# Kernel optimization log

Hardware: AMD Instinct MI355X
Metric: run time of the kernel (lower is better)

The kernel has to match this reference:

```python
import jax, jax.numpy as jnp
import numpy as np

N_NODES = 100_000
N_EDGES = 1_600_000
N_GRAPHS = 64
IN_CH = 128
HID = 64
OUT_CH = 2


def setup_inputs() -> dict:
    key = jax.random.key(0)
    ks = jax.random.split(key, 12)

    def lin(k, fan_in, fan_out):
        s = 1.0 / np.sqrt(fan_in)
        return jax.random.uniform(k, (fan_in, fan_out), jnp.float32, -s, s)

    x = jax.random.normal(ks[0], (N_NODES, IN_CH), jnp.float32)
    edge_index = jax.random.randint(ks[1], (2, N_EDGES), 0, N_NODES, jnp.int64)
    batch = jnp.sort(jax.random.randint(ks[2], (N_NODES,), 0, N_GRAPHS, jnp.int64))
    return {
        "x": x,
        "edge_index": edge_index,
        "batch": batch,
        "w_rel0": lin(ks[3], IN_CH, HID),
        "b_rel0": jnp.zeros((HID,), jnp.float32),
        "w_root0": lin(ks[4], IN_CH, HID),
        "w_rel1": lin(ks[5], HID, HID),
        "b_rel1": jnp.zeros((HID,), jnp.float32),
        "w_root1": lin(ks[6], HID, HID),
        "w_rel2": lin(ks[7], HID, HID),
        "b_rel2": jnp.zeros((HID,), jnp.float32),
        "w_root2": lin(ks[8], HID, HID),
        "head_w1": lin(ks[9], HID, HID),
        "head_b1": jnp.zeros((HID,), jnp.float32),
        "head_w2": lin(ks[10], HID, OUT_CH),
        "head_b2": jnp.zeros((OUT_CH,), jnp.float32),
    }


def _graph_conv(x, src, dst, w_rel, b_rel, w_root):
    # PyG GraphConv: out = lin_rel(sum_{j->i} x_j) + lin_root(x_i)
    agg = jax.ops.segment_sum(x[src], dst, num_segments=N_NODES)  # [N, d_in]
    return agg @ w_rel + b_rel + x @ w_root


def reference(x, edge_index, batch, w_rel0, b_rel0, w_root0,
              w_rel1, b_rel1, w_root1, w_rel2, b_rel2, w_root2,
              head_w1, head_b1, head_w2, head_b2):
    src, dst = edge_index[0], edge_index[1]
    h = jax.nn.relu(_graph_conv(x, src, dst, w_rel0, b_rel0, w_root0))
    h = jax.nn.relu(_graph_conv(h, src, dst, w_rel1, b_rel1, w_root1))
    h = jax.nn.relu(_graph_conv(h, src, dst, w_rel2, b_rel2, w_root2))
    # global_mean_pool over graph ids (dropout is identity at inference)
    sums = jax.ops.segment_sum(h, batch, num_segments=N_GRAPHS)          # [G, H]
    cnts = jax.ops.segment_sum(jnp.ones((N_NODES,), h.dtype), batch,
                               num_segments=N_GRAPHS)                    # [G]
    pooled = sums / jnp.maximum(cnts, 1.0)[:, None]
    z = jax.nn.relu(pooled @ head_w1 + head_b1)
    return z @ head_w2 + head_b2
```

## Files before the change

kernel.cpp:

```cpp
#include <hip/hip_runtime.h>
#include <hip/hip_bf16.h>

#define CAP 64
#define KBUCK 391
#define BSHIFT 8
#define BCAP 4608
#define CHUNK_A 2048
#define AITER (CHUNK_A / 256)
#define LDSZ 36864

typedef __attribute__((ext_vector_type(8))) short short8;
typedef __attribute__((ext_vector_type(4))) float f32x4;

__device__ inline unsigned short bfbits(float f) {
    __hip_bfloat16 b = __float2bfloat16(f);
    unsigned short u;
    __builtin_memcpy(&u, &b, 2);
    return u;
}

__device__ inline void bucket_body(char* smem, int bb, const int* __restrict__ ei,
                                   int E, int* __restrict__ gcur,
                                   unsigned* __restrict__ bucketed)
{
    int* hist = (int*)smem;
    int* base = hist + KBUCK;
    const int e0 = bb * CHUNK_A;
    const int e1 = min(e0 + CHUNK_A, E);
    for (int i = threadIdx.x; i < KBUCK; i += 256) hist[i] = 0;
    __syncthreads();
    int dreg[AITER];
    #pragma unroll
    for (int it = 0; it < AITER; ++it) {
        int e = e0 + it * 256 + threadIdx.x;
        dreg[it] = (e < e1) ? ei[E + e] : -1;
        if (dreg[it] >= 0) atomicAdd(&hist[dreg[it] >> BSHIFT], 1);
    }
    __syncthreads();
    for (int i = threadIdx.x; i < KBUCK; i += 256) {
        int h = hist[i];
        base[i] = h ? atomicAdd(&gcur[i], h) : 0;
        hist[i] = 0;
    }
    __syncthreads();
    #pragma unroll
    for (int it = 0; it < AITER; ++it) {
        int e = e0 + it * 256 + threadIdx.x;
        if (e < e1) {
            int s = ei[e];
            int d = dreg[it];
            int b = d >> BSHIFT;
            int off = base[b] + atomicAdd(&hist[b], 1);
            if (off < BCAP)
                bucketed[(size_t)b * BCAP + off] = ((unsigned)s << 8) | (unsigned)(d & 255);
        }
    }
}

__global__ __launch_bounds__(256) void build_slots_kernel(
    const unsigned* __restrict__ bucketed, const int* __restrict__ gcur,
    int* __restrict__ cnt, int* __restrict__ slots, int N)
{
    __shared__ int lcnt[256];
    const int b = blockIdx.x;
    const int nb0 = b << BSHIFT;
    lcnt[threadIdx.x] = 0;
    __syncthreads();
    const int count = min(gcur[b], BCAP);
    const unsigned* src = bucketed + (size_t)b * BCAP;
    for (int i = threadIdx.x; i < count; i += 256) {
        unsigned p = src[i];
        int dl = (int)(p & 255u);
        int pos = atomicAdd(&lcnt[dl], 1);
        if (pos < CAP) slots[(size_t)(nb0 + dl) * CAP + pos] = (int)(p >> 8);
    }
    __syncthreads();
    int node = nb0 + threadIdx.x;
    if (node < N) cnt[node] = min(lcnt[threadIdx.x], CAP);
}

__global__ __launch_bounds__(256) void prep_weights_kernel(
    const float* __restrict__ wr0, const float* __restrict__ wt0,
    const float* __restrict__ wr1, const float* __restrict__ wt1,
    const float* __restrict__ wr2, const float* __restrict__ wt2,
    __hip_bfloat16* __restrict__ hi, __hip_bfloat16* __restrict__ lo)
{
    int idx = blockIdx.x * 256 + threadIdx.x;
    if (idx >= 32768) return;
    const float *wr, *wt;
    int n, k;
    if (idx < 16384)      { wr = wr0; wt = wt0; int r = idx;         n = r >> 7; k = r & 127; }
    else if (idx < 24576) { wr = wr1; wt = wt1; int r = idx - 16384; n = r >> 6; k = r & 63; }
    else                  { wr = wr2; wt = wt2; int r = idx - 24576; n = r >> 6; k = r & 63; }
    float w = (n < 64) ? wr[k * 64 + n] : wt[k * 64 + (n - 64)];
    __hip_bfloat16 h = __float2bfloat16(w);
    hi[idx] = h;
    lo[idx] = __float2bfloat16(w - __bfloat162float(h));
}

template <int DIN, bool AFP32>
__device__ inline void mfma_body(
    char* smem, int bx, const void* __restrict__ featv,
    const __hip_bfloat16* __restrict__ whiT, const __hip_bfloat16* __restrict__ wloT,
    const float* __restrict__ b_rel,
    __hip_bfloat16* __restrict__ y, __hip_bfloat16* __restrict__ r, int N)
{
    __hip_bfloat16* As = (__hip_bfloat16*)smem;
    __hip_bfloat16* Bh = As + 128 * 48;
    __hip_bfloat16* Bl = Bh + 128 * 48;
    const int t = threadIdx.x;
    const int lane = t & 63;
    const int wid = t >> 6;
    const int wm = wid >> 1, wn = wid & 1;
    const int node0 = bx * 128;
    const int lrow = lane & 15;
    const int kgrp = lane >> 4;

    f32x4 acc[4][4];
    #pragma unroll
    for (int i = 0; i < 4; ++i)
        #pragma unroll
        for (int j = 0; j < 4; ++j) acc[i][j] = (f32x4){0.f, 0.f, 0.f, 0.f};

    for (int ks = 0; ks < DIN / 32; ++ks) {
        #pragma unroll
        for (int p = 0; p < 2; ++p) {
            int c = t + p * 256;
            int m = c >> 2, kc = c & 3;
            int row = node0 + m; if (row >= N) row = N - 1;
            if (AFP32) {
                const float* feat = (const float*)featv;
                const float* src = feat + (size_t)row * DIN + ks * 32 + kc * 8;
                float4 v0 = *(const float4*)src;
                float4 v1 = *(const float4*)(src + 4);
                union { uint4 q; unsigned short s[8]; } pk;
                pk.s[0] = bfbits(v0.x); pk.s[1] = bfbits(v0.y);
                pk.s[2] = bfbits(v0.z); pk.s[3] = bfbits(v0.w);
                pk.s[4] = bfbits(v1.x); pk.s[5] = bfbits(v1.y);
                pk.s[6] = bfbits(v1.z); pk.s[7] = bfbits(v1.w);
                *(uint4*)&As[m * 48 + kc * 8] = pk.q;
            } else {
                const __hip_bfloat16* feat = (const __hip_bfloat16*)featv;
                *(uint4*)&As[m * 48 + kc * 8] =
                    *(const uint4*)(feat + (size_t)row * DIN + ks * 32 + kc * 8);
            }
        }
        #pragma unroll
        for (int p = 0; p < 4; ++p) {
            int c = t + p * 256;
            int half = c >> 9;
            int cc = c & 511;
            int n = cc >> 2, kc = cc & 3;
            const __hip_bfloat16* w = half ? wloT : whiT;
            uint4 v = *(const uint4*)(w + (size_t)n * DIN + ks * 32 + kc * 8);
            if (half) *(uint4*)&Bl[n * 48 + kc * 8] = v;
            else      *(uint4*)&Bh[n * 48 + kc * 8] = v;
        }
        __syncthreads();

        short8 a[4], bh[4], bl[4];
        #pragma unroll
        for (int i = 0; i < 4; ++i)
            a[i] = *(const short8*)&As[(wm * 64 + i * 16 + lrow) * 48 + kgrp * 8];
        #pragma unroll
        for (int j = 0; j < 4; ++j) {
            bh[j] = *(const short8*)&Bh[(wn * 64 + j * 16 + lrow) * 48 + kgrp * 8];
            bl[j] = *(const short8*)&Bl[(wn * 64 + j * 16 + lrow) * 48 + kgrp * 8];
        }
        #pragma unroll
        for (int i = 0; i < 4; ++i)
            #pragma unroll
            for (int j = 0; j < 4; ++j) {
                acc[i][j] = __builtin_amdgcn_mfma_f32_16x16x32_bf16(a[i], bh[j], acc[i][j], 0, 0, 0);
                acc[i][j] = __builtin_amdgcn_mfma_f32_16x16x32_bf16(a[i], bl[j], acc[i][j], 0, 0, 0);
            }
        __syncthreads();
    }

    #pragma unroll
    for (int i = 0; i < 4; ++i) {
        int mbase = node0 + wm * 64 + i * 16 + kgrp * 4;
        #pragma unroll
        for (int j = 0; j < 4; ++j) {
            int n = wn * 64 + j * 16 + lrow;
            #pragma unroll
            for (int v = 0; v < 4; ++v) {
                int m = mbase + v;
                if (m < N) {
                    float val = acc[i][j][v];
                    if (n < 64) y[(size_t)m * 64 + n] = __float2bfloat16(val);
                    else        r[(size_t)m * 64 + (n - 64)] = __float2bfloat16(val + b_rel[n - 64]);
                }
            }
        }
    }
}

__global__ __launch_bounds__(256) void fused_l0_kernel(
    const float* __restrict__ x,
    const __hip_bfloat16* __restrict__ whiT, const __hip_bfloat16* __restrict__ wloT,
    const float* __restrict__ b_rel,
    __hip_bfloat16* __restrict__ y, __hip_bfloat16* __restrict__ r, int N,
    int gemm_blocks, const int* __restrict__ ei, int E,
    int* __restrict__ gcur, unsigned* __restrict__ bucketed)
{
    extern __shared__ char smem[];
    if ((int)blockIdx.x < gemm_blocks)
        mfma_body<128, true>(smem, blockIdx.x, x, whiT, wloT, b_rel, y, r, N);
    else
        bucket_body(smem, blockIdx.x - gemm_blocks, ei, E, gcur, bucketed);
}

template <int DIN>
__global__ __launch_bounds__(256) void mfma_lin_kernel(
    const __hip_bfloat16* __restrict__ feat,
    const __hip_bfloat16* __restrict__ whiT, const __hip_bfloat16* __restrict__ wloT,
    const float* __restrict__ b_rel,
    __hip_bfloat16* __restrict__ y, __hip_bfloat16* __restrict__ r, int N)
{
    extern __shared__ char smem[];
    mfma_body<DIN, false>(smem, blockIdx.x, feat, whiT, wloT, b_rel, y, r, N);
}

__global__ __launch_bounds__(256) void gather_relu_kernel(
    const __hip_bfloat16* __restrict__ y, const int* __restrict__ cnt,
    const int* __restrict__ slots, const __hip_bfloat16* __restrict__ rin,
    __hip_bfloat16* __restrict__ hout, int N)
{
    const int node = blockIdx.x * 8 + (threadIdx.x >> 5);
    if (node >= N) return;
    const int sub = threadIdx.x & 31;
    const int nb = sub >> 3;
    const int ch = (sub & 7) * 8;
    const int deg = cnt[node];
    const int* sl = slots + (size_t)node * CAP;
    const unsigned short* yp = (const unsigned short*)y;

    float a[8], b[8];
    #pragma unroll
    for (int k = 0; k < 8; ++k) { a[k] = 0.f; b[k] = 0.f; }

    #pragma unroll 2
    for (int j = nb; j < deg; j += 8) {
        int n0 = sl[j];
        uint4 v = *(const uint4*)(yp + (size_t)n0 * 64 + ch);
        a[0] += __uint_as_float(v.x << 16); a[1] += __uint_as_float(v.x & 0xffff0000u);
        a[2] += __uint_as_float(v.y << 16); a[3] += __uint_as_float(v.y & 0xffff0000u);
        a[4] += __uint_as_float(v.z << 16); a[5] += __uint_as_float(v.z & 0xffff0000u);
        a[6] += __uint_as_float(v.w << 16); a[7] += __uint_as_float(v.w & 0xffff0000u);
        int j2 = j + 4;
        if (j2 < deg) {
            int n1 = sl[j2];
            uint4 w = *(const uint4*)(yp + (size_t)n1 * 64 + ch);
            b[0] += __uint_as_float(w.x << 16); b[1] += __uint_as_float(w.x & 0xffff0000u);
            b[2] += __uint_as_float(w.y << 16); b[3] += __uint_as_float(w.y & 0xffff0000u);
            b[4] += __uint_as_float(w.z << 16); b[5] += __uint_as_float(w.z & 0xffff0000u);
            b[6] += __uint_as_float(w.w << 16); b[7] += __uint_as_float(w.w & 0xffff0000u);
        }
    }
    #pragma unroll
    for (int k = 0; k < 8; ++k) {
        a[k] += b[k];
        a[k] += __shfl_xor(a[k], 8);
        a[k] += __shfl_xor(a[k], 16);
    }
    if (nb == 0) {
        uint4 rv = *(const uint4*)((const unsigned short*)rin + (size_t)node * 64 + ch);
        float r0 = __uint_as_float(rv.x << 16), r1 = __uint_as_float(rv.x & 0xffff0000u);
        float r2 = __uint_as_float(rv.y << 16), r3 = __uint_as_float(rv.y & 0xffff0000u);
        float r4 = __uint_as_float(rv.z << 16), r5 = __uint_as_float(rv.z & 0xffff0000u);
        float r6 = __uint_as_float(rv.w << 16), r7 = __uint_as_float(rv.w & 0xffff0000u);
        float f0 = fmaxf(r0 + a[0], 0.f), f1 = fmaxf(r1 + a[1], 0.f);
        float f2 = fmaxf(r2 + a[2], 0.f), f3 = fmaxf(r3 + a[3], 0.f);
        float f4 = fmaxf(r4 + a[4], 0.f), f5 = fmaxf(r5 + a[5], 0.f);
        float f6 = fmaxf(r6 + a[6], 0.f), f7 = fmaxf(r7 + a[7], 0.f);
        union { uint4 q; unsigned short s[8]; } pk;
        pk.s[0] = bfbits(f0); pk.s[1] = bfbits(f1); pk.s[2] = bfbits(f2); pk.s[3] = bfbits(f3);
        pk.s[4] = bfbits(f4); pk.s[5] = bfbits(f5); pk.s[6] = bfbits(f6); pk.s[7] = bfbits(f7);
        *(uint4*)((unsigned short*)hout + (size_t)node * 64 + ch) = pk.q;
    }
}

__global__ __launch_bounds__(256) void pool_kernel(
    const __hip_bfloat16* __restrict__ h, const int* __restrict__ batch,
    float* __restrict__ gsum, int* __restrict__ gcnt, int N)
{
    const int CHUNK = 64;
    int wid = (blockIdx.x * 256 + threadIdx.x) >> 6;
    int lane = threadIdx.x & 63;
    int nb = lane >> 3;
    int ch = (lane & 7) * 8;
    int start = wid * CHUNK;
    if (start >= N) return;
    int end = min(start + CHUNK, N);
    const unsigned short* hp = (const unsigned short*)h;

    float a[8];
    #pragma unroll
    for (int k = 0; k < 8; ++k) a[k] = 0.f;
    int runcnt = 0;
    int i = start;
    int gcur = batch[start];

    while (i < end) {
        int idx = i + lane; if (idx > end - 1) idx = end - 1;
        int bl = batch[idx];
        unsigned long long diff = __ballot(bl != gcur && (i + lane) < end);
        int len = diff ? ((int)__ffsll(diff) - 1) : min(64, end - i);
        for (int j = i + nb; j < i + len; j += 8) {
            uint4 v = *(const uint4*)(hp + (size_t)j * 64 + ch);
            a[0] += __uint_as_float(v.x << 16); a[1] += __uint_as_float(v.x & 0xffff0000u);
            a[2] += __uint_as_float(v.y << 16); a[3] += __uint_as_float(v.y & 0xffff0000u);
            a[4] += __uint_as_float(v.z << 16); a[5] += __uint_as_float(v.z & 0xffff0000u);
            a[6] += __uint_as_float(v.w << 16); a[7] += __uint_as_float(v.w & 0xffff0000u);
        }
        runcnt += len;
        i += len;
        if (diff) {
            #pragma unroll
            for (int k = 0; k < 8; ++k) {
                a[k] += __shfl_xor(a[k], 8);
                a[k] += __shfl_xor(a[k], 16);
                a[k] += __shfl_xor(a[k], 32);
            }
            if (runcnt > 0) {
                if (nb == 0) {
                    #pragma unroll
                    for (int k = 0; k < 8; ++k)
                        atomicAdd(&gsum[gcur * 64 + ch + k], a[k]);
                }
                if (lane == 0) atomicAdd(&gcnt[gcur], runcnt);
            }
            #pragma unroll
            for (int k = 0; k < 8; ++k) a[k] = 0.f;
            runcnt = 0;
            gcur = __shfl(bl, len);
        }
    }
    #pragma unroll
    for (int k = 0; k < 8; ++k) {
        a[k] += __shfl_xor(a[k], 8);
        a[k] += __shfl_xor(a[k], 16);
        a[k] += __shfl_xor(a[k], 32);
    }
    if (runcnt > 0) {
        if (nb == 0) {
            #pragma unroll
            for (int k = 0; k < 8; ++k)
                atomicAdd(&gsum[gcur * 64 + ch + k], a[k]);
        }
        if (lane == 0) atomicAdd(&gcnt[gcur], runcnt);
    }
}

__global__ __launch_bounds__(256) void head_kernel(
    const float* __restrict__ gsum, const int* __restrict__ gcnt,
    const float* __restrict__ w1, const float* __restrict__ b1,
    const float* __restrict__ w2, const float* __restrict__ b2,
    float* __restrict__ out)
{
    __shared__ float pm[64 * 64];
    __shared__ float z[64 * 64];
    int t = threadIdx.x;
    for (int i = t; i < 64 * 64; i += 256) {
        int g = i >> 6;
        float cf = (float)gcnt[g];
        if (cf < 1.f) cf = 1.f;
        pm[i] = gsum[i] / cf;
    }
    __syncthreads();
    for (int i = t; i < 64 * 64; i += 256) {
        int g = i >> 6, c = i & 63;
        float a = b1[c];
        #pragma unroll 8
        for (int k = 0; k < 64; ++k) a = fmaf(pm[g * 64 + k], w1[k * 64 + c], a);
        z[i] = fmaxf(a, 0.f);
    }
    __syncthreads();
    for (int i = t; i < 64 * 2; i += 256) {
        int g = i >> 1, o = i & 1;
        float a = b2[o];
        #pragma unroll 8
        for (int k = 0; k < 64; ++k) a = fmaf(z[g * 64 + k], w2[k * 2 + o], a);
        out[i] = a;
    }
}

extern "C" void kernel_launch(void* const* d_in, const int* in_sizes, int n_in,
                              void* d_out, int out_size, void* d_ws, size_t ws_size,
                              hipStream_t stream)
{
    const float* x       = (const float*)d_in[0];
    const int*   ei      = (const int*)d_in[1];
    const int*   batch   = (const int*)d_in[2];
    const float* w_rel0  = (const float*)d_in[3];
    const float* b_rel0  = (const float*)d_in[4];
    const float* w_root0 = (const float*)d_in[5];
    const float* w_rel1  = (const float*)d_in[6];
    const float* b_rel1  = (const float*)d_in[7];
    const float* w_root1 = (const float*)d_in[8];
    const float* w_rel2  = (const float*)d_in[9];
    const float* b_rel2  = (const float*)d_in[10];
    const float* w_root2 = (const float*)d_in[11];
    const float* hw1     = (const float*)d_in[12];
    const float* hb1     = (const float*)d_in[13];
    const float* hw2     = (const float*)d_in[14];
    const float* hb2     = (const float*)d_in[15];
    float* out = (float*)d_out;

    const int N = in_sizes[0] / 128;
    const int E = in_sizes[1] / 2;
    const int G = 64;

    size_t off = 0;
    auto alloc = [&](size_t bytes) -> void* {
        void* p = (char*)d_ws + off;
        off += (bytes + 255) & ~(size_t)255;
        return p;
    };
    int*      cnt      = (int*)alloc((size_t)N * 4);
    int*      slots    = (int*)alloc((size_t)N * CAP * 4);
    unsigned* bucketed = (unsigned*)alloc((size_t)KBUCK * BCAP * 4);
    int*      gcur     = (int*)alloc((size_t)KBUCK * 4);
    __hip_bfloat16* whiT = (__hip_bfloat16*)alloc(32768 * 2);
    __hip_bfloat16* wloT = (__hip_bfloat16*)alloc(32768 * 2);
    __hip_bfloat16* ybf  = (__hip_bfloat16*)alloc((size_t)N * 64 * 2);
    __hip_bfloat16* h0   = (__hip_bfloat16*)alloc((size_t)N * 64 * 2);
    __hip_bfloat16* h1   = (__hip_bfloat16*)alloc((size_t)N * 64 * 2);
    __hip_bfloat16* rbf  = (__hip_bfloat16*)alloc((size_t)N * 64 * 2);
    float* gsum     = (float*)alloc((size_t)G * 64 * 4);
    int*   gcnt     = (int*)alloc((size_t)G * 4);
    (void)ws_size; (void)n_in;

    hipMemsetAsync(gcur, 0, (size_t)KBUCK * 4, stream);
    hipMemsetAsync(gsum, 0, (size_t)G * 64 * 4, stream);
    hipMemsetAsync(gcnt, 0, (size_t)G * 4, stream);

    prep_weights_kernel<<<128, 256, 0, stream>>>(w_rel0, w_root0, w_rel1, w_root1,
                                                 w_rel2, w_root2, whiT, wloT);

    const int gemm_blocks = (N + 127) / 128;
    const int bucket_blocks = (E + CHUNK_A - 1) / CHUNK_A;
    const int gather_blocks = (N + 7) / 8;

    fused_l0_kernel<<<gemm_blocks + bucket_blocks, 256, LDSZ, stream>>>(
        x, whiT, wloT, b_rel0, ybf, rbf, N, gemm_blocks, ei, E, gcur, bucketed);
    build_slots_kernel<<<KBUCK, 256, 0, stream>>>(bucketed, gcur, cnt, slots, N);
    gather_relu_kernel<<<gather_blocks, 256, 0, stream>>>(ybf, cnt, slots, rbf, h0, N);

    mfma_lin_kernel<64><<<gemm_blocks, 256, LDSZ, stream>>>(
        h0, whiT + 16384, wloT + 16384, b_rel1, ybf, rbf, N);
    gather_relu_kernel<<<gather_blocks, 256, 0, stream>>>(ybf, cnt, slots, rbf, h1, N);

    mfma_lin_kernel<64><<<gemm_blocks, 256, LDSZ, stream>>>(
        h1, whiT + 24576, wloT + 24576, b_rel2, ybf, rbf, N);
    gather_relu_kernel<<<gather_blocks, 256, 0, stream>>>(ybf, cnt, slots, rbf, h0, N);

    int pool_waves  = (N + 63) / 64;
    int pool_blocks = (pool_waves + 3) / 4;
    pool_kernel<<<pool_blocks, 256, 0, stream>>>(h0, batch, gsum, gcnt, N);
    head_kernel<<<1, 256, 0, stream>>>(gsum, gcnt, hw1, hb1, hw2, hb2, out);
}
```

Measured before the change: 374.5 us.

## Double-buffer layer-0 GEMM staging, load MFMA operands directly, fold memsets into prep

The layer-0 GEMM now stages only the fp32-to-bf16 converted activations in a double-buffered LDS tile with a smaller stride, prefetching the next K slice while the MFMAs run. Weight fragments are read straight from global memory instead of going through LDS. The layer-1/2 GEMMs drop LDS completely and load both A and B fragments directly from global memory, removing the barriers. The three hipMemsetAsync calls are folded into the weight-prep kernel. The aim is less sync and staging overhead and fewer launches, at the cost of uncoalesced, L2-dependent fragment loads.

```diff
diff --git a/kernel.cpp b/kernel.cpp
--- a/kernel.cpp
+++ b/kernel.cpp
@@ -7,7 +7,8 @@
 #define BCAP 4608
 #define CHUNK_A 2048
 #define AITER (CHUNK_A / 256)
-#define LDSZ 36864
+#define ASTR 40
+#define LDSZ (2 * 128 * ASTR * 2)
 
 typedef __attribute__((ext_vector_type(8))) short short8;
 typedef __attribute__((ext_vector_type(4))) float f32x4;
@@ -17,6 +18,15 @@
     unsigned short u;
     __builtin_memcpy(&u, &b, 2);
     return u;
+}
+
+__device__ inline uint4 pack8(float4 v0, float4 v1) {
+    union { uint4 q; unsigned short s[8]; } pk;
+    pk.s[0] = bfbits(v0.x); pk.s[1] = bfbits(v0.y);
+    pk.s[2] = bfbits(v0.z); pk.s[3] = bfbits(v0.w);
+    pk.s[4] = bfbits(v1.x); pk.s[5] = bfbits(v1.y);
+    pk.s[6] = bfbits(v1.z); pk.s[7] = bfbits(v1.w);
+    return pk.q;
 }
 
 __device__ inline void bucket_body(char* smem, int bb, const int* __restrict__ ei,
@@ -83,9 +93,13 @@
     const float* __restrict__ wr0, const float* __restrict__ wt0,
     const float* __restrict__ wr1, const float* __restrict__ wt1,
     const float* __restrict__ wr2, const float* __restrict__ wt2,
-    __hip_bfloat16* __restrict__ hi, __hip_bfloat16* __restrict__ lo)
+    __hip_bfloat16* __restrict__ hi, __hip_bfloat16* __restrict__ lo,
+    int* __restrict__ gcur, float* __restrict__ gsum, int* __restrict__ gcnt)
 {
     int idx = blockIdx.x * 256 + threadIdx.x;
+    if (idx < KBUCK) gcur[idx] = 0;
+    if (idx < 64 * 64) gsum[idx] = 0.f;
+    if (idx < 64) gcnt[idx] = 0;
     if (idx >= 32768) return;
     const float *wr, *wt;
     int n, k;
@@ -98,85 +112,11 @@
     lo[idx] = __float2bfloat16(w - __bfloat162float(h));
 }
 
-template <int DIN, bool AFP32>
-__device__ inline void mfma_body(
-    char* smem, int bx, const void* __restrict__ featv,
-    const __hip_bfloat16* __restrict__ whiT, const __hip_bfloat16* __restrict__ wloT,
-    const float* __restrict__ b_rel,
-    __hip_bfloat16* __restrict__ y, __hip_bfloat16* __restrict__ r, int N)
-{
-    __hip_bfloat16* As = (__hip_bfloat16*)smem;
-    __hip_bfloat16* Bh = As + 128 * 48;
-    __hip_bfloat16* Bl = Bh + 128 * 48;
-    const int t = threadIdx.x;
-    const int lane = t & 63;
-    const int wid = t >> 6;
-    const int wm = wid >> 1, wn = wid & 1;
-    const int node0 = bx * 128;
-    const int lrow = lane & 15;
-    const int kgrp = lane >> 4;
-
-    f32x4 acc[4][4];
-    #pragma unroll
-    for (int i = 0; i < 4; ++i)
-        #pragma unroll
-        for (int j = 0; j < 4; ++j) acc[i][j] = (f32x4){0.f, 0.f, 0.f, 0.f};
-
-    for (int ks = 0; ks < DIN / 32; ++ks) {
-        #pragma unroll
-        for (int p = 0; p < 2; ++p) {
-            int c = t + p * 256;
-            int m = c >> 2, kc = c & 3;
-            int row = node0 + m; if (row >= N) row = N - 1;
-            if (AFP32) {
-                const float* feat = (const float*)featv;
-                const float* src = feat + (size_t)row * DIN + ks * 32 + kc * 8;
-                float4 v0 = *(const float4*)src;
-                float4 v1 = *(const float4*)(src + 4);
-                union { uint4 q; unsigned short s[8]; } pk;
-                pk.s[0] = bfbits(v0.x); pk.s[1] = bfbits(v0.y);
-                pk.s[2] = bfbits(v0.z); pk.s[3] = bfbits(v0.w);
-                pk.s[4] = bfbits(v1.x); pk.s[5] = bfbits(v1.y);
-                pk.s[6] = bfbits(v1.z); pk.s[7] = bfbits(v1.w);
-                *(uint4*)&As[m * 48 + kc * 8] = pk.q;
-            } else {
-                const __hip_bfloat16* feat = (const __hip_bfloat16*)featv;
-                *(uint4*)&As[m * 48 + kc * 8] =
-                    *(const uint4*)(feat + (size_t)row * DIN + ks * 32 + kc * 8);
-            }
-        }
-        #pragma unroll
-        for (int p = 0; p < 4; ++p) {
-            int c = t + p * 256;
-            int half = c >> 9;
-            int cc = c & 511;
-            int n = cc >> 2, kc = cc & 3;
-            const __hip_bfloat16* w = half ? wloT : whiT;
-            uint4 v = *(const uint4*)(w + (size_t)n * DIN + ks * 32 + kc * 8);
-            if (half) *(uint4*)&Bl[n * 48 + kc * 8] = v;
-            else      *(uint4*)&Bh[n * 48 + kc * 8] = v;
-        }
-        __syncthreads();
-
-        short8 a[4], bh[4], bl[4];
-        #pragma unroll
-        for (int i = 0; i < 4; ++i)
-            a[i] = *(const short8*)&As[(wm * 64 + i * 16 + lrow) * 48 + kgrp * 8];
-        #pragma unroll
-        for (int j = 0; j < 4; ++j) {
-            bh[j] = *(const short8*)&Bh[(wn * 64 + j * 16 + lrow) * 48 + kgrp * 8];
-            bl[j] = *(const short8*)&Bl[(wn * 64 + j * 16 + lrow) * 48 + kgrp * 8];
-        }
-        #pragma unroll
-        for (int i = 0; i < 4; ++i)
-            #pragma unroll
-            for (int j = 0; j < 4; ++j) {
-                acc[i][j] = __builtin_amdgcn_mfma_f32_16x16x32_bf16(a[i], bh[j], acc[i][j], 0, 0, 0);
-                acc[i][j] = __builtin_amdgcn_mfma_f32_16x16x32_bf16(a[i], bl[j], acc[i][j], 0, 0, 0);
-            }
-        __syncthreads();
-    }
-
+__device__ inline void store_cd(f32x4 (&acc)[4][4], int node0, int wm, int wn,
+                                int kgrp, int lrow, const float* __restrict__ b_rel,
+                                __hip_bfloat16* __restrict__ y,
+                                __hip_bfloat16* __restrict__ r, int N)
+{
     #pragma unroll
     for (int i = 0; i < 4; ++i) {
         int mbase = node0 + wm * 64 + i * 16 + kgrp * 4;
@@ -196,6 +136,88 @@
     }
 }
 
+__device__ inline void mfma_l0_body(char* smem, int bx, const float* __restrict__ x,
+    const __hip_bfloat16* __restrict__ whiT, const __hip_bfloat16* __restrict__ wloT,
+    const float* __restrict__ b_rel,
+    __hip_bfloat16* __restrict__ y, __hip_bfloat16* __restrict__ r, int N)
+{
+    __hip_bfloat16* As = (__hip_bfloat16*)smem;
+    const int t = threadIdx.x;
+    const int lane = t & 63;
+    const int wid = t >> 6;
+    const int wm = wid >> 1, wn = wid & 1;
+    const int node0 = bx * 128;
+    const int lrow = lane & 15;
+    const int kgrp = lane >> 4;
+
+    int sm[2], sk[2];
+    const float* sp[2];
+    #pragma unroll
+    for (int p = 0; p < 2; ++p) {
+        int c = t + p * 256;
+        sm[p] = c >> 2;
+        sk[p] = (c & 3) * 8;
+        int row = node0 + sm[p]; if (row >= N) row = N - 1;
+        sp[p] = x + (size_t)row * 128 + sk[p];
+    }
+
+    f32x4 acc[4][4];
+    #pragma unroll
+    for (int i = 0; i < 4; ++i)
+        #pragma unroll
+        for (int j = 0; j < 4; ++j) acc[i][j] = (f32x4){0.f, 0.f, 0.f, 0.f};
+
+    #pragma unroll
+    for (int p = 0; p < 2; ++p) {
+        float4 v0 = *(const float4*)(sp[p]);
+        float4 v1 = *(const float4*)(sp[p] + 4);
+        *(uint4*)&As[sm[p] * ASTR + sk[p]] = pack8(v0, v1);
+    }
+    __syncthreads();
+
+    #pragma unroll
+    for (int ks = 0; ks < 4; ++ks) {
+        const int buf  = (ks & 1) * (128 * ASTR);
+        const int nbuf = ((ks + 1) & 1) * (128 * ASTR);
+
+        float4 nv0[2], nv1[2];
+        if (ks < 3) {
+            #pragma unroll
+            for (int p = 0; p < 2; ++p) {
+                nv0[p] = *(const float4*)(sp[p] + (ks + 1) * 32);
+                nv1[p] = *(const float4*)(sp[p] + (ks + 1) * 32 + 4);
+            }
+        }
+
+        short8 a[4], bh[4], bl[4];
+        #pragma unroll
+        for (int i = 0; i < 4; ++i)
+            a[i] = *(const short8*)&As[buf + (wm * 64 + i * 16 + lrow) * ASTR + kgrp * 8];
+        #pragma unroll
+        for (int j = 0; j < 4; ++j) {
+            int n = wn * 64 + j * 16 + lrow;
+            bh[j] = *(const short8*)(whiT + (size_t)n * 128 + ks * 32 + kgrp * 8);
+            bl[j] = *(const short8*)(wloT + (size_t)n * 128 + ks * 32 + kgrp * 8);
+        }
+        #pragma unroll
+        for (int i = 0; i < 4; ++i)
+            #pragma unroll
+            for (int j = 0; j < 4; ++j) {
+                acc[i][j] = __builtin_amdgcn_mfma_f32_16x16x32_bf16(a[i], bh[j], acc[i][j], 0, 0, 0);
+                acc[i][j] = __builtin_amdgcn_mfma_f32_16x16x32_bf16(a[i], bl[j], acc[i][j], 0, 0, 0);
+            }
+
+        if (ks < 3) {
+            #pragma unroll
+            for (int p = 0; p < 2; ++p)
+                *(uint4*)&As[nbuf + sm[p] * ASTR + sk[p]] = pack8(nv0[p], nv1[p]);
+        }
+        __syncthreads();
+    }
+
+    store_cd(acc, node0, wm, wn, kgrp, lrow, b_rel, y, r, N);
+}
+
 __global__ __launch_bounds__(256) void fused_l0_kernel(
     const float* __restrict__ x,
     const __hip_bfloat16* __restrict__ whiT, const __hip_bfloat16* __restrict__ wloT,
@@ -206,7 +228,7 @@
 {
     extern __shared__ char smem[];
     if ((int)blockIdx.x < gemm_blocks)
-        mfma_body<128, true>(smem, blockIdx.x, x, whiT, wloT, b_rel, y, r, N);
+        mfma_l0_body(smem, blockIdx.x, x, whiT, wloT, b_rel, y, r, N);
     else
         bucket_body(smem, blockIdx.x - gemm_blocks, ei, E, gcur, bucketed);
 }
@@ -218,8 +240,45 @@
     const float* __restrict__ b_rel,
     __hip_bfloat16* __restrict__ y, __hip_bfloat16* __restrict__ r, int N)
 {
-    extern __shared__ char smem[];
-    mfma_body<DIN, false>(smem, blockIdx.x, feat, whiT, wloT, b_rel, y, r, N);
+    const int t = threadIdx.x;
+    const int lane = t & 63;
+    const int wid = t >> 6;
+    const int wm = wid >> 1, wn = wid & 1;
+    const int node0 = blockIdx.x * 128;
+    const int lrow = lane & 15;
+    const int kgrp = lane >> 4;
+
+    f32x4 acc[4][4];
+    #pragma unroll
+    for (int i = 0; i < 4; ++i)
+        #pragma unroll
+        for (int j = 0; j < 4; ++j) acc[i][j] = (f32x4){0.f, 0.f, 0.f, 0.f};
+
+    #pragma unroll
+    for (int ks = 0; ks < DIN / 32; ++ks) {
+        short8 a[4], bh[4], bl[4];
+        #pragma unroll
+        for (int i = 0; i < 4; ++i) {
+            int row = node0 + wm * 64 + i * 16 + lrow;
+            if (row >= N) row = N - 1;
+            a[i] = *(const short8*)(feat + (size_t)row * DIN + ks * 32 + kgrp * 8);
+        }
+        #pragma unroll
+        for (int j = 0; j < 4; ++j) {
+            int n = wn * 64 + j * 16 + lrow;
+            bh[j] = *(const short8*)(whiT + (size_t)n * DIN + ks * 32 + kgrp * 8);
+            bl[j] = *(const short8*)(wloT + (size_t)n * DIN + ks * 32 + kgrp * 8);
+        }
+        #pragma unroll
+        for (int i = 0; i < 4; ++i)
+            #pragma unroll
+            for (int j = 0; j < 4; ++j) {
+                acc[i][j] = __builtin_amdgcn_mfma_f32_16x16x32_bf16(a[i], bh[j], acc[i][j], 0, 0, 0);
+                acc[i][j] = __builtin_amdgcn_mfma_f32_16x16x32_bf16(a[i], bl[j], acc[i][j], 0, 0, 0);
+            }
+    }
+
+    store_cd(acc, node0, wm, wn, kgrp, lrow, b_rel, y, r, N);
 }
 
 __global__ __launch_bounds__(256) void gather_relu_kernel(
@@ -432,12 +491,9 @@
     int*   gcnt     = (int*)alloc((size_t)G * 4);
     (void)ws_size; (void)n_in;
 
-    hipMemsetAsync(gcur, 0, (size_t)KBUCK * 4, stream);
-    hipMemsetAsync(gsum, 0, (size_t)G * 64 * 4, stream);
-    hipMemsetAsync(gcnt, 0, (size_t)G * 4, stream);
-
     prep_weights_kernel<<<128, 256, 0, stream>>>(w_rel0, w_root0, w_rel1, w_root1,
-                                                 w_rel2, w_root2, whiT, wloT);
+                                                 w_rel2, w_root2, whiT, wloT,
+                                                 gcur, gsum, gcnt);
 
     const int gemm_blocks = (N + 127) / 128;
     const int bucket_blocks = (E + CHUNK_A - 1) / CHUNK_A;
@@ -448,11 +504,11 @@
     build_slots_kernel<<<KBUCK, 256, 0, stream>>>(bucketed, gcur, cnt, slots, N);
     gather_relu_kernel<<<gather_blocks, 256, 0, stream>>>(ybf, cnt, slots, rbf, h0, N);
 
-    mfma_lin_kernel<64><<<gemm_blocks, 256, LDSZ, stream>>>(
+    mfma_lin_kernel<64><<<gemm_blocks, 256, 0, stream>>>(
         h0, whiT + 16384, wloT + 16384, b_rel1, ybf, rbf, N);
     gather_relu_kernel<<<gather_blocks, 256, 0, stream>>>(ybf, cnt, slots, rbf, h1, N);
 
-    mfma_lin_kernel<64><<<gemm_blocks, 256, LDSZ, stream>>>(
+    mfma_lin_kernel<64><<<gemm_blocks, 256, 0, stream>>>(
         h1, whiT + 24576, wloT + 24576, b_rel2, ybf, rbf, N);
     gather_relu_kernel<<<gather_blocks, 256, 0, stream>>>(ybf, cnt, slots, rbf, h0, N);
 
```

New measurement: 391.0 us. 1.04x slower.
